# Optimization experiments

Hardware: AMD Instinct MI355X
Metric: run time of the kernel (lower is better)

## Reference

```python
import jax, jax.numpy as jnp
import numpy as np

N = 50000    # total nodes in a batched graph
E = 200000   # directed edges (before self loops)
G = 256      # molecules per batch
F_IN = 64    # atom features
H = 4        # gat heads
CH = 128     # hidden_channels (per head)
D = H * CH   # 512, concat width
MLP_H = 128  # hidden_channels * mlp_hidden_factor
NEG_SLOPE = 0.2


def _gat(x, src, dst, W, a_src, a_dst, b, concat):
    """PyG GATConv (eval mode, self loops already added to src/dst)."""
    n = x.shape[0]
    heads, ch = a_src.shape
    h = (x @ W).reshape(n, heads, ch)                       # [N,H,C]
    e = jax.nn.leaky_relu((h * a_src).sum(-1)[src]
                          + (h * a_dst).sum(-1)[dst], NEG_SLOPE)  # [E,H]
    emax = jax.ops.segment_max(e, dst, num_segments=n)
    emax = jnp.where(jnp.isfinite(emax), emax, 0.0)
    p = jnp.exp(e - emax[dst])
    denom = jax.ops.segment_sum(p, dst, num_segments=n)
    alpha = p / (denom[dst] + 1e-16)                        # segment softmax over dst
    out = jax.ops.segment_sum(h[src] * alpha[..., None], dst, num_segments=n)
    out = out.reshape(n, heads * ch) if concat else out.mean(axis=1)
    return out + b


def _encoder(x, edge_index, batch, p):
    n = x.shape[0]
    loop = jnp.arange(n, dtype=edge_index.dtype)            # GATConv add_self_loops=True
    src = jnp.concatenate([edge_index[0], loop])
    dst = jnp.concatenate([edge_index[1], loop])
    x = jax.nn.elu(_gat(x, src, dst, p['W1'], p['as1'], p['ad1'], p['b1'], True))
    x = jax.nn.elu(_gat(x, src, dst, p['W2'], p['as2'], p['ad2'], p['b2'], True))
    x = _gat(x, src, dst, p['W3'], p['as3'], p['ad3'], p['b3'], False)
    emb = jax.ops.segment_max(x, batch, num_segments=G)     # global_max_pool
    return jnp.where(jnp.isfinite(emb), emb, 0.0)


def setup_inputs() -> dict:
    key = jax.random.key(0)
    ks = jax.random.split(key, 24)
    rn = lambda k, s, sc=0.1: jax.random.normal(k, s, jnp.float32) * sc
    return dict(
        x1=rn(ks[0], (N, F_IN), 1.0),
        edge_index1=jax.random.randint(ks[1], (2, E), 0, N, dtype=jnp.int32),
        batch1=jnp.sort(jax.random.randint(ks[2], (N,), 0, G, dtype=jnp.int32)),
        x2=rn(ks[3], (N, F_IN), 1.0),
        edge_index2=jax.random.randint(ks[4], (2, E), 0, N, dtype=jnp.int32),
        batch2=jnp.sort(jax.random.randint(ks[5], (N,), 0, G, dtype=jnp.int32)),
        W1=rn(ks[6], (F_IN, D)), as1=rn(ks[7], (H, CH)), ad1=rn(ks[8], (H, CH)),
        b1=jnp.zeros((D,), jnp.float32),
        W2=rn(ks[9], (D, D)), as2=rn(ks[10], (H, CH)), ad2=rn(ks[11], (H, CH)),
        b2=jnp.zeros((D,), jnp.float32),
        W3=rn(ks[12], (D, CH)), as3=rn(ks[13], (1, CH)), ad3=rn(ks[14], (1, CH)),
        b3=jnp.zeros((CH,), jnp.float32),
        mw1=rn(ks[15], (2 * CH, MLP_H)), mb1=jnp.zeros((MLP_H,), jnp.float32),
        mw2=rn(ks[16], (MLP_H, 1)), mb2=jnp.zeros((1,), jnp.float32),
    )


def reference(x1, edge_index1, batch1, x2, edge_index2, batch2,
              W1, as1, ad1, b1, W2, as2, ad2, b2, W3, as3, ad3, b3,
              mw1, mb1, mw2, mb2):
    p = dict(W1=W1, as1=as1, ad1=ad1, b1=b1,
             W2=W2, as2=as2, ad2=ad2, b2=b2,
             W3=W3, as3=as3, ad3=ad3, b3=b3)
    e1 = _encoder(x1, edge_index1, batch1, p)               # [G, CH]
    e2 = _encoder(x2, edge_index2, batch2, p)               # [G, CH]
    z = jnp.concatenate([e1, e2], axis=-1)                  # [G, 2*CH]
    return jax.nn.relu(z @ mw1 + mb1) @ mw2 + mb2           # [G, 1]
```

## Files before the change

### kernel.cpp

```cpp
#include <hip/hip_runtime.h>
#include <cstdint>

namespace {
constexpr int kN = 50000;
constexpr int kE = 200000;
constexpr int kE2 = kE + kN;
constexpr int kG = 256;
constexpr float kNegSlope = 0.2f;
}

using half8   = __attribute__((ext_vector_type(8))) _Float16;
using floatx4 = __attribute__((ext_vector_type(4))) float;

__device__ __forceinline__ void gld_lds16(const void* g, void* l) {
  __builtin_amdgcn_global_load_lds(
      (const __attribute__((address_space(1))) unsigned int*)g,
      (__attribute__((address_space(3))) unsigned int*)l, 16, 0, 0);
}

__device__ __forceinline__ float fexp(float x) {
  return __builtin_amdgcn_exp2f(x * 1.44269504088896f);
}

template <int OUTF16, int BN, int CT>
__global__ __launch_bounds__(512, 2) void gemm_ring(
    const _Float16* __restrict__ A, const _Float16* __restrict__ B,
    void* __restrict__ Cv, int M, int N, int K) {
  constexpr int ASL = 1024;
  constexpr int BSL = BN * 4;
  constexpr int SLOT = (ASL + BSL) * 16;
  constexpr int LPT = (ASL + BSL) / 512;
  constexpr int WN = (BN == 256) ? 4 : 2;
  constexpr int WM = 8 / WN;
  constexpr int WTM = 256 / WM;
  constexpr int WTN = BN / WN;
  constexpr int MI = WTM / 16;
  constexpr int NI = WTN / 16;
  __shared__ alignas(16) char smem[4 * SLOT];
  const int t = threadIdx.x;
  const int w = t >> 6, l = t & 63;
  const int x = blockIdx.x & 7, s = blockIdx.x >> 3;
  const int col = (CT == 1) ? 0 : (s & (CT - 1));
  const int rt = ((CT == 1) ? s : (s >> 1)) * 8 + x;
  const int bm = rt * 256;
  const int bn = col * BN;
  if (bm >= M) return;
  const int wr = w / WN, wc = w % WN;
  const int quad = l >> 4, lrow = l & 15;

  floatx4 acc[MI][NI];
#pragma unroll
  for (int mi = 0; mi < MI; ++mi)
#pragma unroll
    for (int ni = 0; ni < NI; ++ni) acc[mi][ni] = (floatx4){0.f, 0.f, 0.f, 0.f};

  auto stageA = [&](int kt) {
    char* buf = smem + (size_t)(kt & 3) * SLOT;
    int k0 = kt * 32;
    k0 = (k0 > K - 32) ? (K - 32) : k0;
#pragma unroll
    for (int i = 0; i < 2; ++i) {
      const int sl = i * 512 + t;
      const int row = ((sl >> 6) << 4) + (sl & 15);
      const int q = (sl >> 4) & 3;
      int ga = bm + row;
      ga = (ga < M) ? ga : (M - 1);
      gld_lds16(A + (size_t)ga * K + k0 + q * 8, buf + sl * 16);
    }
  };
  auto stageB = [&](int kt) {
    char* buf = smem + (size_t)(kt & 3) * SLOT + ASL * 16;
    int k0 = kt * 32;
    k0 = (k0 > K - 32) ? (K - 32) : k0;
#pragma unroll
    for (int i = 0; i < LPT - 2; ++i) {
      const int sl = i * 512 + t;
      const int row = ((sl >> 6) << 4) + (sl & 15);
      const int q = (sl >> 4) & 3;
      gld_lds16(B + (size_t)(bn + row) * K + k0 + q * 8, buf + sl * 16);
    }
  };

  stageA(0); stageB(0);
  stageA(1); stageB(1);
  stageA(2); stageB(2);

  const int NT = K >> 5;
  for (int kt = 0; kt < NT; ++kt) {
    char* bufc = smem + (size_t)(kt & 3) * SLOT;
    stageA(kt + 3);
    if constexpr (BN == 256)
      asm volatile("s_waitcnt vmcnt(10)" ::: "memory");
    else
      asm volatile("s_waitcnt vmcnt(8)" ::: "memory");
    __builtin_amdgcn_s_barrier();
    asm volatile("" ::: "memory");
    half8 fa[MI], fb[NI];
#pragma unroll
    for (int ni = 0; ni < NI; ++ni)
      fb[ni] = *(const half8*)(bufc + ASL * 16 + ((wc * NI + ni) << 10) + l * 16);
#pragma unroll
    for (int mi = 0; mi < MI / 2; ++mi)
      fa[mi] = *(const half8*)(bufc + ((wr * MI + mi) << 10) + l * 16);
    __builtin_amdgcn_s_setprio(1);
#pragma unroll
    for (int mi = 0; mi < MI / 2; ++mi)
#pragma unroll
      for (int ni = 0; ni < NI; ++ni)
        acc[mi][ni] = __builtin_amdgcn_mfma_f32_16x16x32_f16(
            fa[mi], fb[ni], acc[mi][ni], 0, 0, 0);
    __builtin_amdgcn_s_setprio(0);
    stageB(kt + 3);
#pragma unroll
    for (int mi = MI / 2; mi < MI; ++mi)
      fa[mi] = *(const half8*)(bufc + ((wr * MI + mi) << 10) + l * 16);
    __builtin_amdgcn_s_setprio(1);
#pragma unroll
    for (int mi = MI / 2; mi < MI; ++mi)
#pragma unroll
      for (int ni = 0; ni < NI; ++ni)
        acc[mi][ni] = __builtin_amdgcn_mfma_f32_16x16x32_f16(
            fa[mi], fb[ni], acc[mi][ni], 0, 0, 0);
    __builtin_amdgcn_s_setprio(0);
    asm volatile("" ::: "memory");
    __builtin_amdgcn_s_barrier();
  }
  asm volatile("s_waitcnt vmcnt(0)" ::: "memory");
  const int colbase = bn + wc * WTN + lrow;
#pragma unroll
  for (int mi = 0; mi < MI; ++mi) {
    const int rbase = bm + wr * WTM + mi * 16 + quad * 4;
#pragma unroll
    for (int r = 0; r < 4; ++r) {
      const int grow = rbase + r;
      if (grow < M) {
        if constexpr (OUTF16) {
          _Float16* C = (_Float16*)Cv;
#pragma unroll
          for (int ni = 0; ni < NI; ++ni)
            C[(size_t)grow * N + colbase + ni * 16] = (_Float16)acc[mi][ni][r];
        } else {
          float* C = (float*)Cv;
#pragma unroll
          for (int ni = 0; ni < NI; ++ni)
            C[(size_t)grow * N + colbase + ni * 16] = acc[mi][ni][r];
        }
      }
    }
  }
}

__global__ void wt_split_all(const float* __restrict__ W1, _Float16* Th1,
                             const float* __restrict__ W2, _Float16* Th2,
                             const float* __restrict__ W3, _Float16* Th3) {
  int idx = blockIdx.x * blockDim.x + threadIdx.x;
  const float* W;
  _Float16* Th;
  int K, N;
  if (idx < 64 * 512) {
    W = W1; Th = Th1; K = 64; N = 512;
  } else if (idx < 64 * 512 + 512 * 512) {
    idx -= 64 * 512;
    W = W2; Th = Th2; K = 512; N = 512;
  } else if (idx < 64 * 512 + 512 * 512 + 512 * 128) {
    idx -= 64 * 512 + 512 * 512;
    W = W3; Th = Th3; K = 512; N = 128;
  } else {
    return;
  }
  const int k = idx / N;
  const int n = idx - k * N;
  Th[n * K + k] = (_Float16)W[idx];
}

__global__ void prep2(const float* __restrict__ x0, const float* __restrict__ x1,
                      _Float16* __restrict__ Xh, int* __restrict__ cnt,
                      int* __restrict__ total) {
  const int idx = blockIdx.x * blockDim.x + threadIdx.x;
  const int half = kN * 64;
  if (idx < half) Xh[idx] = (_Float16)x0[idx];
  else if (idx < 2 * half) Xh[idx] = (_Float16)x1[idx - half];
  if (idx < 2 * kN) cnt[idx] = 1;
  if (idx == 0) *total = 0;
}
__global__ void prep(const float* __restrict__ X, _Float16* __restrict__ Xh,
                     int* __restrict__ cnt, int* __restrict__ total, int nsplit,
                     int n) {
  const int idx = blockIdx.x * blockDim.x + threadIdx.x;
  if (idx < nsplit) Xh[idx] = (_Float16)X[idx];
  if (idx < n) cnt[idx] = 1;
  if (idx == 0) *total = 0;
}

__global__ void count_edges2(const int* __restrict__ d0, const int* __restrict__ d1,
                             int* __restrict__ cnt) {
  const int i = blockIdx.x * blockDim.x + threadIdx.x;
  if (i < kE) atomicAdd(&cnt[d0[i]], 1);
  else if (i < 2 * kE) atomicAdd(&cnt[d1[i - kE] + kN], 1);
}
__global__ void fill_edges2(const int* __restrict__ s0, const int* __restrict__ d0,
                            const int* __restrict__ s1, const int* __restrict__ d1,
                            int* __restrict__ cursor, int* __restrict__ csr) {
  const int i = blockIdx.x * blockDim.x + threadIdx.x;
  if (i < kE) {
    const int p = atomicAdd(&cursor[d0[i]], 1);
    csr[p] = s0[i];
  } else if (i < 2 * kE) {
    const int j = i - kE;
    const int p = atomicAdd(&cursor[d1[j] + kN], 1);
    csr[p] = s1[j] + kN;
  }
}
__global__ void count_edges(const int* __restrict__ dst, int* __restrict__ cnt,
                            int ne) {
  const int i = blockIdx.x * blockDim.x + threadIdx.x;
  if (i < ne) atomicAdd(&cnt[dst[i]], 1);
}
__global__ void fill_edges(const int* __restrict__ src, const int* __restrict__ dst,
                           int* __restrict__ cursor, int* __restrict__ csr, int ne) {
  const int i = blockIdx.x * blockDim.x + threadIdx.x;
  if (i < ne) {
    const int p = atomicAdd(&cursor[dst[i]], 1);
    csr[p] = src[i];
  }
}
__global__ void alloc_ranges(const int* __restrict__ cnt, int* __restrict__ start,
                             int* __restrict__ cursor, int* __restrict__ total,
                             int* __restrict__ csr, int n) {
  const int i = blockIdx.x * blockDim.x + threadIdx.x;
  const int lane = threadIdx.x & 63;
  const int v = (i < n) ? cnt[i] : 0;
  int sc = v;
#pragma unroll
  for (int off = 1; off < 64; off <<= 1) {
    const int t = __shfl_up(sc, off);
    if (lane >= off) sc += t;
  }
  const int wtot = __shfl(sc, 63);
  int base = 0;
  if (lane == 63) base = atomicAdd(total, wtot);
  base = __shfl(base, 63);
  const int st = base + sc - v;
  if (i < n) {
    start[i] = st;
    cursor[i] = st + 1;
    csr[st] = i;
  }
}

__global__ void gat_agg4(const _Float16* __restrict__ h,
                         const float* __restrict__ a_src,
                         const float* __restrict__ a_dst,
                         const int* __restrict__ start, const int* __restrict__ cnt,
                         const int* __restrict__ csr_src,
                         const float* __restrict__ bias,
                         _Float16* __restrict__ outH, int n_nodes) {
  const int gtid = blockIdx.x * blockDim.x + threadIdx.x;
  const int node = gtid >> 6;
  const int lane = threadIdx.x & 63;
  if (node >= n_nodes) return;
  const int ch = lane * 8;
  float as_r[8], ad_r[8];
#pragma unroll
  for (int j = 0; j < 8; ++j) {
    as_r[j] = a_src[ch + j];
    ad_r[j] = a_dst[ch + j];
  }
  const int s = start[node];
  const int c = cnt[node];
  const half8 vs = *(const half8*)(h + (size_t)node * 512 + ch);
  float fs[8];
  float t_src = 0.f, t_dst = 0.f;
#pragma unroll
  for (int j = 0; j < 8; ++j) {
    fs[j] = (float)vs[j];
    t_src = fmaf(fs[j], as_r[j], t_src);
    t_dst = fmaf(fs[j], ad_r[j], t_dst);
  }
#pragma unroll
  for (int off = 1; off < 16; off <<= 1) {
    t_src += __shfl_xor(t_src, off);
    t_dst += __shfl_xor(t_dst, off);
  }
  const float ad = t_dst;
  float es = t_src + ad;
  es = (es > 0.f) ? es : kNegSlope * es;
  const float ws = fexp(es);
  float d0 = ws, d1 = 0.f;
  float a0[8], a1[8];
#pragma unroll
  for (int j = 0; j < 8; ++j) {
    a0[j] = ws * fs[j];
    a1[j] = 0.f;
  }
  int i = 1;
  for (; i + 2 <= c; i += 2) {
    const int s0 = csr_src[s + i];
    const int s1 = csr_src[s + i + 1];
    const half8 v0 = *(const half8*)(h + (size_t)s0 * 512 + ch);
    const half8 v1 = *(const half8*)(h + (size_t)s1 * 512 + ch);
    float f0[8], f1[8];
    float t0 = 0.f, t1 = 0.f;
#pragma unroll
    for (int j = 0; j < 8; ++j) {
      f0[j] = (float)v0[j];
      f1[j] = (float)v1[j];
      t0 = fmaf(f0[j], as_r[j], t0);
      t1 = fmaf(f1[j], as_r[j], t1);
    }
#pragma unroll
    for (int off = 1; off < 16; off <<= 1) {
      t0 += __shfl_xor(t0, off);
      t1 += __shfl_xor(t1, off);
    }
    float e0 = t0 + ad;
    float e1 = t1 + ad;
    e0 = (e0 > 0.f) ? e0 : kNegSlope * e0;
    e1 = (e1 > 0.f) ? e1 : kNegSlope * e1;
    const float w0 = fexp(e0);
    const float w1 = fexp(e1);
    d0 += w0;
    d1 += w1;
#pragma unroll
    for (int j = 0; j < 8; ++j) {
      a0[j] = fmaf(w0, f0[j], a0[j]);
      a1[j] = fmaf(w1, f1[j], a1[j]);
    }
  }
  if (i < c) {
    const int s0 = csr_src[s + i];
    const half8 v0 = *(const half8*)(h + (size_t)s0 * 512 + ch);
    float f0[8];
    float t0 = 0.f;
#pragma unroll
    for (int j = 0; j < 8; ++j) {
      f0[j] = (float)v0[j];
      t0 = fmaf(f0[j], as_r[j], t0);
    }
#pragma unroll
    for (int off = 1; off < 16; off <<= 1) t0 += __shfl_xor(t0, off);
    float e0 = t0 + ad;
    e0 = (e0 > 0.f) ? e0 : kNegSlope * e0;
    const float w0 = fexp(e0);
    d0 += w0;
#pragma unroll
    for (int j = 0; j < 8; ++j) a0[j] = fmaf(w0, f0[j], a0[j]);
  }
  const float inv = 1.f / (d0 + d1 + 1e-16f);
  half8 H;
#pragma unroll
  for (int j = 0; j < 8; ++j) {
    float v = (a0[j] + a1[j]) * inv + bias[ch + j];
    v = (v > 0.f) ? v : (fexp(v) - 1.f);
    H[j] = (_Float16)v;
  }
  *(half8*)(outH + (size_t)node * 512 + ch) = H;
}

__global__ void gat_agg_l3(const float* __restrict__ h,
                           const float* __restrict__ a_src,
                           const float* __restrict__ a_dst,
                           const int* __restrict__ start, const int* __restrict__ cnt,
                           const int* __restrict__ csr_src,
                           const float* __restrict__ bias,
                           float* __restrict__ out, int n_nodes) {
  const int gtid = blockIdx.x * blockDim.x + threadIdx.x;
  const int node = gtid >> 6;
  const int lane = threadIdx.x & 63;
  if (node >= n_nodes) return;
  const float2 asv = *(const float2*)(a_src + lane * 2);
  const float2 adv = *(const float2*)(a_dst + lane * 2);
  const int s = start[node];
  const int c = cnt[node];
  const float2 vs = *(const float2*)(h + (size_t)node * 128 + lane * 2);
  float t_src = fmaf(vs.x, asv.x, vs.y * asv.y);
  float t_dst = fmaf(vs.x, adv.x, vs.y * adv.y);
#pragma unroll
  for (int off = 1; off < 64; off <<= 1) {
    t_src += __shfl_xor(t_src, off);
    t_dst += __shfl_xor(t_dst, off);
  }
  const float ad = t_dst;
  float es = t_src + ad;
  es = (es > 0.f) ? es : kNegSlope * es;
  const float ws = fexp(es);
  float2 a0 = make_float2(ws * vs.x, ws * vs.y);
  float2 a1 = make_float2(0.f, 0.f);
  float d0 = ws, d1 = 0.f;
  int i = 1;
  for (; i + 2 <= c; i += 2) {
    const int s0 = csr_src[s + i];
    const int s1 = csr_src[s + i + 1];
    const float2 v0 = *(const float2*)(h + (size_t)s0 * 128 + lane * 2);
    const float2 v1 = *(const float2*)(h + (size_t)s1 * 128 + lane * 2);
    float t0 = fmaf(v0.x, asv.x, v0.y * asv.y);
    float t1 = fmaf(v1.x, asv.x, v1.y * asv.y);
#pragma unroll
    for (int off = 1; off < 64; off <<= 1) {
      t0 += __shfl_xor(t0, off);
      t1 += __shfl_xor(t1, off);
    }
    float e0 = t0 + ad;
    float e1 = t1 + ad;
    e0 = (e0 > 0.f) ? e0 : kNegSlope * e0;
    e1 = (e1 > 0.f) ? e1 : kNegSlope * e1;
    const float w0 = fexp(e0);
    const float w1 = fexp(e1);
    d0 += w0;
    d1 += w1;
    a0.x = fmaf(w0, v0.x, a0.x); a1.x = fmaf(w1, v1.x, a1.x);
    a0.y = fmaf(w0, v0.y, a0.y); a1.y = fmaf(w1, v1.y, a1.y);
  }
  if (i < c) {
    const int s0 = csr_src[s + i];
    const float2 v0 = *(const float2*)(h + (size_t)s0 * 128 + lane * 2);
    float t0 = fmaf(v0.x, asv.x, v0.y * asv.y);
#pragma unroll
    for (int off = 1; off < 64; off <<= 1) t0 += __shfl_xor(t0, off);
    float e0 = t0 + ad;
    e0 = (e0 > 0.f) ? e0 : kNegSlope * e0;
    const float w0 = fexp(e0);
    d0 += w0;
    a0.x = fmaf(w0, v0.x, a0.x);
    a0.y = fmaf(w0, v0.y, a0.y);
  }
  const float inv = 1.f / (d0 + d1 + 1e-16f);
  *(float2*)(out + (size_t)node * 128 + lane * 2) =
      make_float2((a0.x + a1.x) * inv + bias[lane * 2],
                  (a0.y + a1.y) * inv + bias[lane * 2 + 1]);
}

__global__ void pool_max2(const float* __restrict__ x, const int* __restrict__ bt1,
                          const int* __restrict__ bt2, float* __restrict__ emb) {
  __shared__ int lohi[2];
  const int enc = blockIdx.x >> 8;
  const int g = blockIdx.x & 255;
  const int* batch = enc ? bt2 : bt1;
  const float* xx = x + (size_t)enc * kN * 128;
  if (threadIdx.x == 0) {
    int lo = 0, hi = kN;
    while (lo < hi) {
      const int mid = (lo + hi) >> 1;
      if (batch[mid] < g) lo = mid + 1; else hi = mid;
    }
    lohi[0] = lo;
    hi = kN;
    while (lo < hi) {
      const int mid = (lo + hi) >> 1;
      if (batch[mid] < g + 1) lo = mid + 1; else hi = mid;
    }
    lohi[1] = lo;
  }
  __syncthreads();
  const int lo = lohi[0], hi = lohi[1];
  const int c = threadIdx.x;
  float m = -1e30f;
  for (int nid = lo; nid < hi; ++nid) m = fmaxf(m, xx[(size_t)nid * 128 + c]);
  emb[(size_t)blockIdx.x * 128 + c] = (lo < hi) ? m : 0.f;
}
__global__ void pool_max(const float* __restrict__ x, const int* __restrict__ batch,
                         float* __restrict__ emb, int n_nodes) {
  __shared__ int lohi[2];
  const int g = blockIdx.x;
  if (threadIdx.x == 0) {
    int lo = 0, hi = n_nodes;
    while (lo < hi) {
      const int mid = (lo + hi) >> 1;
      if (batch[mid] < g) lo = mid + 1; else hi = mid;
    }
    lohi[0] = lo;
    hi = n_nodes;
    while (lo < hi) {
      const int mid = (lo + hi) >> 1;
      if (batch[mid] < g + 1) lo = mid + 1; else hi = mid;
    }
    lohi[1] = lo;
  }
  __syncthreads();
  const int lo = lohi[0], hi = lohi[1];
  const int c = threadIdx.x;
  float m = -1e30f;
  for (int nid = lo; nid < hi; ++nid) m = fmaxf(m, x[(size_t)nid * 128 + c]);
  emb[g * 128 + c] = (lo < hi) ? m : 0.f;
}

__global__ void mlp_head(const float* __restrict__ e1, const float* __restrict__ e2,
                         const float* __restrict__ mw1, const float* __restrict__ mb1,
                         const float* __restrict__ mw2, const float* __restrict__ mb2,
                         float* __restrict__ out) {
  __shared__ float z[256];
  __shared__ float red[128];
  const int g = blockIdx.x;
  const int j = threadIdx.x;
  z[j] = e1[g * 128 + j];
  z[j + 128] = e2[g * 128 + j];
  __syncthreads();
  float acc = mb1[j];
  for (int k = 0; k < 256; ++k) acc = fmaf(z[k], mw1[k * 128 + j], acc);
  acc = fmaxf(acc, 0.f) * mw2[j];
  red[j] = acc;
  __syncthreads();
  for (int s = 64; s > 0; s >>= 1) {
    if (j < s) red[j] += red[j + s];
    __syncthreads();
  }
  if (j == 0) out[g] = red[0] + mb2[0];
}

namespace {
struct Bufs {
  _Float16 *R1h, *R2h;
  float *R1f, *R2f, *asrc, *adst;
  int *cnt, *start, *cursor, *csr, *total;
  _Float16 *Wth1, *Wth2, *Wth3;
  float* emb;
  size_t need;
};

Bufs plan(void* d_ws, int M, int E) {
  Bufs b;
  char* w = (char*)d_ws;
  size_t off = 0;
  auto take = [&](size_t bytes) -> void* {
    void* p = w + off;
    off += (bytes + 255) & ~(size_t)255;
    return p;
  };
  b.R1h = (_Float16*)take((size_t)M * 512 * 2);
  b.R1f = (float*)b.R1h;
  b.R2h = (_Float16*)take((size_t)M * 512 * 2);
  b.R2f = (float*)b.R2h;
  b.asrc = (float*)take((size_t)M * 4 * 4);
  b.adst = (float*)take((size_t)M * 4 * 4);
  b.cnt = (int*)take((size_t)M * 4);
  b.start = (int*)take((size_t)M * 4);
  b.cursor = (int*)take((size_t)M * 4);
  b.csr = (int*)take((size_t)E * 4);
  b.total = (int*)take(256);
  b.Wth1 = (_Float16*)take((size_t)64 * 512 * 2);
  b.Wth2 = (_Float16*)take((size_t)512 * 512 * 2);
  b.Wth3 = (_Float16*)take((size_t)512 * 128 * 2);
  b.emb = (float*)take((size_t)2 * kG * 128 * 4);
  b.need = off;
  return b;
}

void run_layers(const Bufs& b, void* const* d_in, int M, hipStream_t stream) {
  const float* as1 = (const float*)d_in[7];
  const float* ad1 = (const float*)d_in[8];
  const float* b1 = (const float*)d_in[9];
  const float* as2 = (const float*)d_in[11];
  const float* ad2 = (const float*)d_in[12];
  const float* b2 = (const float*)d_in[13];
  const float* as3 = (const float*)d_in[15];
  const float* ad3 = (const float*)d_in[16];
  const float* b3 = (const float*)d_in[17];
  const int nodeBlocks = (M * 64) / 256;
  const int MT = (M + 255) / 256;
  const int SP = (MT + 7) / 8;

  gemm_ring<1, 256, 2><<<SP * 16, 512, 0, stream>>>(b.R1h, b.Wth1, b.R2h, M, 512, 64);
  gat_agg4<<<nodeBlocks, 256, 0, stream>>>(b.R2h, as1, ad1, b.start, b.cnt,
                                           b.csr, b1, b.R1h, M);
  gemm_ring<1, 256, 2><<<SP * 16, 512, 0, stream>>>(b.R1h, b.Wth2, b.R2h, M, 512, 512);
  gat_agg4<<<nodeBlocks, 256, 0, stream>>>(b.R2h, as2, ad2, b.start, b.cnt,
                                           b.csr, b2, b.R1h, M);
  gemm_ring<0, 128, 1><<<SP * 8, 512, 0, stream>>>(b.R1h, b.Wth3, b.R2f, M, 128, 512);
  gat_agg_l3<<<nodeBlocks, 256, 0, stream>>>(b.R2f, as3, ad3, b.start, b.cnt,
                                             b.csr, b3, b.R1f, M);
}
}

extern "C" void kernel_launch(void* const* d_in, const int* in_sizes, int n_in,
                              void* d_out, int out_size, void* d_ws, size_t ws_size,
                              hipStream_t stream) {
  (void)in_sizes; (void)n_in; (void)out_size;
  const float* W1 = (const float*)d_in[6];
  const float* W2 = (const float*)d_in[10];
  const float* W3 = (const float*)d_in[14];
  const float* mw1 = (const float*)d_in[18];
  const float* mb1 = (const float*)d_in[19];
  const float* mw2 = (const float*)d_in[20];
  const float* mb2 = (const float*)d_in[21];

  Bufs bc = plan(d_ws, 2 * kN, 2 * kE2);
  const bool combined = bc.need <= ws_size;
  Bufs b = combined ? bc : plan(d_ws, kN, kE2);

  const int wtot = 64 * 512 + 512 * 512 + 512 * 128;
  wt_split_all<<<(wtot + 255) / 256, 256, 0, stream>>>(W1, b.Wth1, W2, b.Wth2, W3,
                                                       b.Wth3);
  if (combined) {
    const int M = 2 * kN;
    const int* ei0 = (const int*)d_in[1];
    const int* ei1 = (const int*)d_in[4];
    prep2<<<(2 * kN * 64 + 255) / 256, 256, 0, stream>>>(
        (const float*)d_in[0], (const float*)d_in[3], b.R1h, b.cnt, b.total);
    count_edges2<<<(2 * kE + 255) / 256, 256, 0, stream>>>(ei0 + kE, ei1 + kE,
                                                           b.cnt);
    alloc_ranges<<<(M + 255) / 256, 256, 0, stream>>>(b.cnt, b.start, b.cursor,
                                                      b.total, b.csr, M);
    fill_edges2<<<(2 * kE + 255) / 256, 256, 0, stream>>>(ei0, ei0 + kE, ei1,
                                                          ei1 + kE, b.cursor, b.csr);
    run_layers(b, d_in, M, stream);
    pool_max2<<<2 * kG, 128, 0, stream>>>(b.R1f, (const int*)d_in[2],
                                          (const int*)d_in[5], b.emb);
  } else {
    for (int enc = 0; enc < 2; ++enc) {
      const float* x = (const float*)d_in[enc * 3 + 0];
      const int* ei = (const int*)d_in[enc * 3 + 1];
      const int* batch = (const int*)d_in[enc * 3 + 2];
      prep<<<(kN * 64 + 255) / 256, 256, 0, stream>>>(x, b.R1h, b.cnt, b.total,
                                                      kN * 64, kN);
      count_edges<<<(kE + 255) / 256, 256, 0, stream>>>(ei + kE, b.cnt, kE);
      alloc_ranges<<<(kN + 255) / 256, 256, 0, stream>>>(b.cnt, b.start, b.cursor,
                                                         b.total, b.csr, kN);
      fill_edges<<<(kE + 255) / 256, 256, 0, stream>>>(ei, ei + kE, b.cursor, b.csr,
                                                       kE);
      run_layers(b, d_in, kN, stream);
      pool_max<<<kG, 128, 0, stream>>>(b.R1f, batch, b.emb + (size_t)enc * kG * 128,
                                       kN);
    }
  }
  mlp_head<<<kG, 128, 0, stream>>>(b.emb, b.emb + (size_t)kG * 128, mw1, mb1, mw2,
                                   mb2, (float*)d_out);
}
```

Measured before the change: 671.9 us.

## Process two nodes per wave in GAT aggregation, fp16 layer-3 features, fuse weight prep

The aggregation kernels now handle two destination nodes per wavefront, interleaving their neighbour gathers so more independent loads are in flight. The masked iteration runs to the larger degree of the pair, so the shorter node issues dummy loads. Layer 3's GEMM now writes fp16 instead of fp32, which halves the gather traffic in the final aggregation at some precision cost. The weight transpose/convert is folded into the input prep kernel to save a launch.

Result: faster. 642.5 us (-4.4%).

```diff
diff --git a/kernel.cpp b/kernel.cpp
--- a/kernel.cpp
+++ b/kernel.cpp
@@ -10,6 +10,7 @@
 }
 
 using half8   = __attribute__((ext_vector_type(8))) _Float16;
+using half2v  = __attribute__((ext_vector_type(2))) _Float16;
 using floatx4 = __attribute__((ext_vector_type(4))) float;
 
 __device__ __forceinline__ void gld_lds16(const void* g, void* l) {
@@ -173,13 +174,40 @@
   Th[n * K + k] = (_Float16)W[idx];
 }
 
-__global__ void prep2(const float* __restrict__ x0, const float* __restrict__ x1,
-                      _Float16* __restrict__ Xh, int* __restrict__ cnt,
-                      int* __restrict__ total) {
+__global__ void prep_all(const float* __restrict__ x0, const float* __restrict__ x1,
+                         _Float16* __restrict__ Xh, int* __restrict__ cnt,
+                         int* __restrict__ total,
+                         const float* __restrict__ W1, _Float16* Th1,
+                         const float* __restrict__ W2, _Float16* Th2,
+                         const float* __restrict__ W3, _Float16* Th3) {
   const int idx = blockIdx.x * blockDim.x + threadIdx.x;
   const int half = kN * 64;
-  if (idx < half) Xh[idx] = (_Float16)x0[idx];
-  else if (idx < 2 * half) Xh[idx] = (_Float16)x1[idx - half];
+  if (idx < half) {
+    Xh[idx] = (_Float16)x0[idx];
+  } else if (idx < 2 * half) {
+    Xh[idx] = (_Float16)x1[idx - half];
+  } else {
+    int e = idx - 2 * half;
+    const float* W;
+    _Float16* Th;
+    int K, N;
+    if (e < 64 * 512) {
+      W = W1; Th = Th1; K = 64; N = 512;
+    } else if (e < 64 * 512 + 512 * 512) {
+      e -= 64 * 512;
+      W = W2; Th = Th2; K = 512; N = 512;
+    } else if (e < 64 * 512 + 512 * 512 + 512 * 128) {
+      e -= 64 * 512 + 512 * 512;
+      W = W3; Th = Th3; K = 512; N = 128;
+    } else {
+      W = nullptr; Th = nullptr; K = N = 0;
+    }
+    if (W) {
+      const int k = e / N;
+      const int n = e - k * N;
+      Th[n * K + k] = (_Float16)W[e];
+    }
+  }
   if (idx < 2 * kN) cnt[idx] = 1;
   if (idx == 0) *total = 0;
 }
@@ -256,9 +284,12 @@
                          const float* __restrict__ bias,
                          _Float16* __restrict__ outH, int n_nodes) {
   const int gtid = blockIdx.x * blockDim.x + threadIdx.x;
-  const int node = gtid >> 6;
+  const int wid = gtid >> 6;
   const int lane = threadIdx.x & 63;
-  if (node >= n_nodes) return;
+  const int n0 = wid * 2;
+  if (n0 >= n_nodes) return;
+  const int n1r = (n0 + 1 < n_nodes) ? (n0 + 1) : n0;
+  const bool has1 = (n0 + 1 < n_nodes);
   const int ch = lane * 8;
   float as_r[8], ad_r[8];
 #pragma unroll
@@ -266,98 +297,140 @@
     as_r[j] = a_src[ch + j];
     ad_r[j] = a_dst[ch + j];
   }
-  const int s = start[node];
-  const int c = cnt[node];
-  const half8 vs = *(const half8*)(h + (size_t)node * 512 + ch);
-  float fs[8];
-  float t_src = 0.f, t_dst = 0.f;
+  const int s0 = start[n0], c0 = cnt[n0];
+  const int s1 = start[n1r];
+  const int c1 = has1 ? cnt[n1r] : 0;
+  const half8 vsA = *(const half8*)(h + (size_t)n0 * 512 + ch);
+  const half8 vsB = *(const half8*)(h + (size_t)n1r * 512 + ch);
+  float fsA[8], fsB[8];
+  float tAs = 0.f, tAd = 0.f, tBs = 0.f, tBd = 0.f;
 #pragma unroll
   for (int j = 0; j < 8; ++j) {
-    fs[j] = (float)vs[j];
-    t_src = fmaf(fs[j], as_r[j], t_src);
-    t_dst = fmaf(fs[j], ad_r[j], t_dst);
+    fsA[j] = (float)vsA[j];
+    fsB[j] = (float)vsB[j];
+    tAs = fmaf(fsA[j], as_r[j], tAs);
+    tAd = fmaf(fsA[j], ad_r[j], tAd);
+    tBs = fmaf(fsB[j], as_r[j], tBs);
+    tBd = fmaf(fsB[j], ad_r[j], tBd);
   }
 #pragma unroll
   for (int off = 1; off < 16; off <<= 1) {
-    t_src += __shfl_xor(t_src, off);
-    t_dst += __shfl_xor(t_dst, off);
-  }
-  const float ad = t_dst;
-  float es = t_src + ad;
-  es = (es > 0.f) ? es : kNegSlope * es;
-  const float ws = fexp(es);
-  float d0 = ws, d1 = 0.f;
-  float a0[8], a1[8];
+    tAs += __shfl_xor(tAs, off);
+    tAd += __shfl_xor(tAd, off);
+    tBs += __shfl_xor(tBs, off);
+    tBd += __shfl_xor(tBd, off);
+  }
+  const float adA = tAd, adB = tBd;
+  float eA = tAs + adA, eB = tBs + adB;
+  eA = (eA > 0.f) ? eA : kNegSlope * eA;
+  eB = (eB > 0.f) ? eB : kNegSlope * eB;
+  const float wsA = fexp(eA);
+  const float wsB = fexp(eB);
+  float dA = wsA, dB = wsB;
+  float aA[8], aB[8];
 #pragma unroll
   for (int j = 0; j < 8; ++j) {
-    a0[j] = ws * fs[j];
-    a1[j] = 0.f;
-  }
+    aA[j] = wsA * fsA[j];
+    aB[j] = wsB * fsB[j];
+  }
+  const int cm = (c0 > c1) ? c0 : c1;
   int i = 1;
-  for (; i + 2 <= c; i += 2) {
-    const int s0 = csr_src[s + i];
-    const int s1 = csr_src[s + i + 1];
-    const half8 v0 = *(const half8*)(h + (size_t)s0 * 512 + ch);
-    const half8 v1 = *(const half8*)(h + (size_t)s1 * 512 + ch);
-    float f0[8], f1[8];
-    float t0 = 0.f, t1 = 0.f;
+  for (; i + 2 <= cm; i += 2) {
+    const int jA0 = (i < c0) ? i : 0, jA1 = (i + 1 < c0) ? i + 1 : 0;
+    const int jB0 = (i < c1) ? i : 0, jB1 = (i + 1 < c1) ? i + 1 : 0;
+    const int sA0 = csr_src[s0 + jA0];
+    const int sA1 = csr_src[s0 + jA1];
+    const int sB0 = csr_src[s1 + jB0];
+    const int sB1 = csr_src[s1 + jB1];
+    const half8 vA0 = *(const half8*)(h + (size_t)sA0 * 512 + ch);
+    const half8 vA1 = *(const half8*)(h + (size_t)sA1 * 512 + ch);
+    const half8 vB0 = *(const half8*)(h + (size_t)sB0 * 512 + ch);
+    const half8 vB1 = *(const half8*)(h + (size_t)sB1 * 512 + ch);
+    float fA0[8], fA1[8], fB0[8], fB1[8];
+    float tA0 = 0.f, tA1 = 0.f, tB0 = 0.f, tB1 = 0.f;
 #pragma unroll
     for (int j = 0; j < 8; ++j) {
-      f0[j] = (float)v0[j];
-      f1[j] = (float)v1[j];
-      t0 = fmaf(f0[j], as_r[j], t0);
-      t1 = fmaf(f1[j], as_r[j], t1);
+      fA0[j] = (float)vA0[j]; tA0 = fmaf(fA0[j], as_r[j], tA0);
+      fA1[j] = (float)vA1[j]; tA1 = fmaf(fA1[j], as_r[j], tA1);
+      fB0[j] = (float)vB0[j]; tB0 = fmaf(fB0[j], as_r[j], tB0);
+      fB1[j] = (float)vB1[j]; tB1 = fmaf(fB1[j], as_r[j], tB1);
     }
 #pragma unroll
     for (int off = 1; off < 16; off <<= 1) {
-      t0 += __shfl_xor(t0, off);
-      t1 += __shfl_xor(t1, off);
-    }
-    float e0 = t0 + ad;
-    float e1 = t1 + ad;
-    e0 = (e0 > 0.f) ? e0 : kNegSlope * e0;
-    e1 = (e1 > 0.f) ? e1 : kNegSlope * e1;
-    const float w0 = fexp(e0);
-    const float w1 = fexp(e1);
-    d0 += w0;
-    d1 += w1;
+      tA0 += __shfl_xor(tA0, off);
+      tA1 += __shfl_xor(tA1, off);
+      tB0 += __shfl_xor(tB0, off);
+      tB1 += __shfl_xor(tB1, off);
+    }
+    float eA0 = tA0 + adA, eA1 = tA1 + adA;
+    float eB0 = tB0 + adB, eB1 = tB1 + adB;
+    eA0 = (eA0 > 0.f) ? eA0 : kNegSlope * eA0;
+    eA1 = (eA1 > 0.f) ? eA1 : kNegSlope * eA1;
+    eB0 = (eB0 > 0.f) ? eB0 : kNegSlope * eB0;
+    eB1 = (eB1 > 0.f) ? eB1 : kNegSlope * eB1;
+    const float wA0 = (i < c0) ? fexp(eA0) : 0.f;
+    const float wA1 = (i + 1 < c0) ? fexp(eA1) : 0.f;
+    const float wB0 = (i < c1) ? fexp(eB0) : 0.f;
+    const float wB1 = (i + 1 < c1) ? fexp(eB1) : 0.f;
+    dA += wA0 + wA1;
+    dB += wB0 + wB1;
 #pragma unroll
     for (int j = 0; j < 8; ++j) {
-      a0[j] = fmaf(w0, f0[j], a0[j]);
-      a1[j] = fmaf(w1, f1[j], a1[j]);
-    }
-  }
-  if (i < c) {
-    const int s0 = csr_src[s + i];
-    const half8 v0 = *(const half8*)(h + (size_t)s0 * 512 + ch);
-    float f0[8];
-    float t0 = 0.f;
+      aA[j] = fmaf(wA0, fA0[j], aA[j]);
+      aA[j] = fmaf(wA1, fA1[j], aA[j]);
+      aB[j] = fmaf(wB0, fB0[j], aB[j]);
+      aB[j] = fmaf(wB1, fB1[j], aB[j]);
+    }
+  }
+  if (i < cm) {
+    const int jA = (i < c0) ? i : 0;
+    const int jB = (i < c1) ? i : 0;
+    const int sA = csr_src[s0 + jA];
+    const int sB = csr_src[s1 + jB];
+    const half8 vA = *(const half8*)(h + (size_t)sA * 512 + ch);
+    const half8 vB = *(const half8*)(h + (size_t)sB * 512 + ch);
+    float fA[8], fB[8];
+    float tA = 0.f, tB = 0.f;
 #pragma unroll
     for (int j = 0; j < 8; ++j) {
-      f0[j] = (float)v0[j];
-      t0 = fmaf(f0[j], as_r[j], t0);
-    }
-#pragma unroll
-    for (int off = 1; off < 16; off <<= 1) t0 += __shfl_xor(t0, off);
-    float e0 = t0 + ad;
-    e0 = (e0 > 0.f) ? e0 : kNegSlope * e0;
-    const float w0 = fexp(e0);
-    d0 += w0;
-#pragma unroll
-    for (int j = 0; j < 8; ++j) a0[j] = fmaf(w0, f0[j], a0[j]);
-  }
-  const float inv = 1.f / (d0 + d1 + 1e-16f);
-  half8 H;
+      fA[j] = (float)vA[j]; tA = fmaf(fA[j], as_r[j], tA);
+      fB[j] = (float)vB[j]; tB = fmaf(fB[j], as_r[j], tB);
+    }
+#pragma unroll
+    for (int off = 1; off < 16; off <<= 1) {
+      tA += __shfl_xor(tA, off);
+      tB += __shfl_xor(tB, off);
+    }
+    float eA2 = tA + adA, eB2 = tB + adB;
+    eA2 = (eA2 > 0.f) ? eA2 : kNegSlope * eA2;
+    eB2 = (eB2 > 0.f) ? eB2 : kNegSlope * eB2;
+    const float wA = (i < c0) ? fexp(eA2) : 0.f;
+    const float wB = (i < c1) ? fexp(eB2) : 0.f;
+    dA += wA;
+    dB += wB;
+#pragma unroll
+    for (int j = 0; j < 8; ++j) {
+      aA[j] = fmaf(wA, fA[j], aA[j]);
+      aB[j] = fmaf(wB, fB[j], aB[j]);
+    }
+  }
+  const float invA = 1.f / (dA + 1e-16f);
+  const float invB = 1.f / (dB + 1e-16f);
+  half8 HA, HB;
 #pragma unroll
   for (int j = 0; j < 8; ++j) {
-    float v = (a0[j] + a1[j]) * inv + bias[ch + j];
-    v = (v > 0.f) ? v : (fexp(v) - 1.f);
-    H[j] = (_Float16)v;
-  }
-  *(half8*)(outH + (size_t)node * 512 + ch) = H;
-}
-
-__global__ void gat_agg_l3(const float* __restrict__ h,
+    float vA = aA[j] * invA + bias[ch + j];
+    vA = (vA > 0.f) ? vA : (fexp(vA) - 1.f);
+    HA[j] = (_Float16)vA;
+    float vB = aB[j] * invB + bias[ch + j];
+    vB = (vB > 0.f) ? vB : (fexp(vB) - 1.f);
+    HB[j] = (_Float16)vB;
+  }
+  *(half8*)(outH + (size_t)n0 * 512 + ch) = HA;
+  if (has1) *(half8*)(outH + (size_t)n1r * 512 + ch) = HB;
+}
+
+__global__ void gat_agg_l3(const _Float16* __restrict__ h,
                            const float* __restrict__ a_src,
                            const float* __restrict__ a_dst,
                            const int* __restrict__ start, const int* __restrict__ cnt,
@@ -365,69 +438,123 @@
                            const float* __restrict__ bias,
                            float* __restrict__ out, int n_nodes) {
   const int gtid = blockIdx.x * blockDim.x + threadIdx.x;
-  const int node = gtid >> 6;
+  const int wid = gtid >> 6;
   const int lane = threadIdx.x & 63;
-  if (node >= n_nodes) return;
+  const int n0 = wid * 2;
+  if (n0 >= n_nodes) return;
+  const int n1r = (n0 + 1 < n_nodes) ? (n0 + 1) : n0;
+  const bool has1 = (n0 + 1 < n_nodes);
   const float2 asv = *(const float2*)(a_src + lane * 2);
   const float2 adv = *(const float2*)(a_dst + lane * 2);
-  const int s = start[node];
-  const int c = cnt[node];
-  const float2 vs = *(const float2*)(h + (size_t)node * 128 + lane * 2);
-  float t_src = fmaf(vs.x, asv.x, vs.y * asv.y);
-  float t_dst = fmaf(vs.x, adv.x, vs.y * adv.y);
+  const int s0 = start[n0], c0 = cnt[n0];
+  const int s1 = start[n1r];
+  const int c1 = has1 ? cnt[n1r] : 0;
+  const half2v vsA = *(const half2v*)(h + (size_t)n0 * 128 + lane * 2);
+  const half2v vsB = *(const half2v*)(h + (size_t)n1r * 128 + lane * 2);
+  const float xA = (float)vsA[0], yA = (float)vsA[1];
+  const float xB = (float)vsB[0], yB = (float)vsB[1];
+  float tAs = fmaf(xA, asv.x, yA * asv.y);
+  float tAd = fmaf(xA, adv.x, yA * adv.y);
+  float tBs = fmaf(xB, asv.x, yB * asv.y);
+  float tBd = fmaf(xB, adv.x, yB * adv.y);
 #pragma unroll
   for (int off = 1; off < 64; off <<= 1) {
-    t_src += __shfl_xor(t_src, off);
-    t_dst += __shfl_xor(t_dst, off);
-  }
-  const float ad = t_dst;
-  float es = t_src + ad;
-  es = (es > 0.f) ? es : kNegSlope * es;
-  const float ws = fexp(es);
-  float2 a0 = make_float2(ws * vs.x, ws * vs.y);
-  float2 a1 = make_float2(0.f, 0.f);
-  float d0 = ws, d1 = 0.f;
+    tAs += __shfl_xor(tAs, off);
+    tAd += __shfl_xor(tAd, off);
+    tBs += __shfl_xor(tBs, off);
+    tBd += __shfl_xor(tBd, off);
+  }
+  const float adA = tAd, adB = tBd;
+  float eA = tAs + adA, eB = tBs + adB;
+  eA = (eA > 0.f) ? eA : kNegSlope * eA;
+  eB = (eB > 0.f) ? eB : kNegSlope * eB;
+  const float wsA = fexp(eA);
+  const float wsB = fexp(eB);
+  float dA = wsA, dB = wsB;
+  float2 aA = make_float2(wsA * xA, wsA * yA);
+  float2 aB = make_float2(wsB * xB, wsB * yB);
+  const int cm = (c0 > c1) ? c0 : c1;
   int i = 1;
-  for (; i + 2 <= c; i += 2) {
-    const int s0 = csr_src[s + i];
-    const int s1 = csr_src[s + i + 1];
-    const float2 v0 = *(const float2*)(h + (size_t)s0 * 128 + lane * 2);
-    const float2 v1 = *(const float2*)(h + (size_t)s1 * 128 + lane * 2);
-    float t0 = fmaf(v0.x, asv.x, v0.y * asv.y);
-    float t1 = fmaf(v1.x, asv.x, v1.y * asv.y);
+  for (; i + 2 <= cm; i += 2) {
+    const int jA0 = (i < c0) ? i : 0, jA1 = (i + 1 < c0) ? i + 1 : 0;
+    const int jB0 = (i < c1) ? i : 0, jB1 = (i + 1 < c1) ? i + 1 : 0;
+    const int sA0 = csr_src[s0 + jA0];
+    const int sA1 = csr_src[s0 + jA1];
+    const int sB0 = csr_src[s1 + jB0];
+    const int sB1 = csr_src[s1 + jB1];
+    const half2v vA0 = *(const half2v*)(h + (size_t)sA0 * 128 + lane * 2);
+    const half2v vA1 = *(const half2v*)(h + (size_t)sA1 * 128 + lane * 2);
+    const half2v vB0 = *(const half2v*)(h + (size_t)sB0 * 128 + lane * 2);
+    const half2v vB1 = *(const half2v*)(h + (size_t)sB1 * 128 + lane * 2);
+    const float xA0 = (float)vA0[0], yA0 = (float)vA0[1];
+    const float xA1 = (float)vA1[0], yA1 = (float)vA1[1];
+    const float xB0 = (float)vB0[0], yB0 = (float)vB0[1];
+    const float xB1 = (float)vB1[0], yB1 = (float)vB1[1];
+    float tA0 = fmaf(xA0, asv.x, yA0 * asv.y);
+    float tA1 = fmaf(xA1, asv.x, yA1 * asv.y);
+    float tB0 = fmaf(xB0, asv.x, yB0 * asv.y);
+    float tB1 = fmaf(xB1, asv.x, yB1 * asv.y);
 #pragma unroll
     for (int off = 1; off < 64; off <<= 1) {
-      t0 += __shfl_xor(t0, off);
-      t1 += __shfl_xor(t1, off);
-    }
-    float e0 = t0 + ad;
-    float e1 = t1 + ad;
-    e0 = (e0 > 0.f) ? e0 : kNegSlope * e0;
-    e1 = (e1 > 0.f) ? e1 : kNegSlope * e1;
-    const float w0 = fexp(e0);
-    const float w1 = fexp(e1);
-    d0 += w0;
-    d1 += w1;
-    a0.x = fmaf(w0, v0.x, a0.x); a1.x = fmaf(w1, v1.x, a1.x);
-    a0.y = fmaf(w0, v0.y, a0.y); a1.y = fmaf(w1, v1.y, a1.y);
-  }
-  if (i < c) {
-    const int s0 = csr_src[s + i];
-    const float2 v0 = *(const float2*)(h + (size_t)s0 * 128 + lane * 2);
-    float t0 = fmaf(v0.x, asv.x, v0.y * asv.y);
-#pragma unroll
-    for (int off = 1; off < 64; off <<= 1) t0 += __shfl_xor(t0, off);
-    float e0 = t0 + ad;
-    e0 = (e0 > 0.f) ? e0 : kNegSlope * e0;
-    const float w0 = fexp(e0);
-    d0 += w0;
-    a0.x = fmaf(w0, v0.x, a0.x);
-    a0.y = fmaf(w0, v0.y, a0.y);
-  }
-  const float inv = 1.f / (d0 + d1 + 1e-16f);
-  *(float2*)(out + (size_t)node * 128 + lane * 2) =
-      make_float2((a0.x + a1.x) * inv + bias[lane * 2],
-                  (a0.y + a1.y) * inv + bias[lane * 2 + 1]);
+      tA0 += __shfl_xor(tA0, off);
+      tA1 += __shfl_xor(tA1, off);
+      tB0 += __shfl_xor(tB0, off);
+      tB1 += __shfl_xor(tB1, off);
+    }
+    float eA0 = tA0 + adA, eA1 = tA1 + adA;
+    float eB0 = tB0 + adB, eB1 = tB1 + adB;
+    eA0 = (eA0 > 0.f) ? eA0 : kNegSlope * eA0;
+    eA1 = (eA1 > 0.f) ? eA1 : kNegSlope * eA1;
+    eB0 = (eB0 > 0.f) ? eB0 : kNegSlope * eB0;
+    eB1 = (eB1 > 0.f) ? eB1 : kNegSlope * eB1;
+    const float wA0 = (i < c0) ? fexp(eA0) : 0.f;
+    const float wA1 = (i + 1 < c0) ? fexp(eA1) : 0.f;
+    const float wB0 = (i < c1) ? fexp(eB0) : 0.f;
+    const float wB1 = (i + 1 < c1) ? fexp(eB1) : 0.f;
+    dA += wA0 + wA1;
+    dB += wB0 + wB1;
+    aA.x = fmaf(wA0, xA0, aA.x); aA.x = fmaf(wA1, xA1, aA.x);
+    aA.y = fmaf(wA0, yA0, aA.y); aA.y = fmaf(wA1, yA1, aA.y);
+    aB.x = fmaf(wB0, xB0, aB.x); aB.x = fmaf(wB1, xB1, aB.x);
+    aB.y = fmaf(wB0, yB0, aB.y); aB.y = fmaf(wB1, yB1, aB.y);
+  }
+  if (i < cm) {
+    const int jA = (i < c0) ? i : 0;
+    const int jB = (i < c1) ? i : 0;
+    const int sA = csr_src[s0 + jA];
+    const int sB = csr_src[s1 + jB];
+    const half2v vA = *(const half2v*)(h + (size_t)sA * 128 + lane * 2);
+    const half2v vB = *(const half2v*)(h + (size_t)sB * 128 + lane * 2);
+    const float xA2 = (float)vA[0], yA2 = (float)vA[1];
+    const float xB2 = (float)vB[0], yB2 = (float)vB[1];
+    float tA = fmaf(xA2, asv.x, yA2 * asv.y);
+    float tB = fmaf(xB2, asv.x, yB2 * asv.y);
+#pragma unroll
+    for (int off = 1; off < 64; off <<= 1) {
+      tA += __shfl_xor(tA, off);
+      tB += __shfl_xor(tB, off);
+    }
+    float eA2 = tA + adA, eB2 = tB + adB;
+    eA2 = (eA2 > 0.f) ? eA2 : kNegSlope * eA2;
+    eB2 = (eB2 > 0.f) ? eB2 : kNegSlope * eB2;
+    const float wA = (i < c0) ? fexp(eA2) : 0.f;
+    const float wB = (i < c1) ? fexp(eB2) : 0.f;
+    dA += wA;
+    dB += wB;
+    aA.x = fmaf(wA, xA2, aA.x);
+    aA.y = fmaf(wA, yA2, aA.y);
+    aB.x = fmaf(wB, xB2, aB.x);
+    aB.y = fmaf(wB, yB2, aB.y);
+  }
+  const float invA = 1.f / (dA + 1e-16f);
+  const float invB = 1.f / (dB + 1e-16f);
+  *(float2*)(out + (size_t)n0 * 128 + lane * 2) =
+      make_float2(aA.x * invA + bias[lane * 2],
+                  aA.y * invA + bias[lane * 2 + 1]);
+  if (has1)
+    *(float2*)(out + (size_t)n1r * 128 + lane * 2) =
+        make_float2(aB.x * invB + bias[lane * 2],
+                    aB.y * invB + bias[lane * 2 + 1]);
 }
 
 __global__ void pool_max2(const float* __restrict__ x, const int* __restrict__ bt1,
@@ -555,19 +682,19 @@
   const float* as3 = (const float*)d_in[15];
   const float* ad3 = (const float*)d_in[16];
   const float* b3 = (const float*)d_in[17];
-  const int nodeBlocks = (M * 64) / 256;
+  const int aggBlocks = (((M + 1) / 2) * 64 + 255) / 256;
   const int MT = (M + 255) / 256;
   const int SP = (MT + 7) / 8;
 
   gemm_ring<1, 256, 2><<<SP * 16, 512, 0, stream>>>(b.R1h, b.Wth1, b.R2h, M, 512, 64);
-  gat_agg4<<<nodeBlocks, 256, 0, stream>>>(b.R2h, as1, ad1, b.start, b.cnt,
-                                           b.csr, b1, b.R1h, M);
+  gat_agg4<<<aggBlocks, 256, 0, stream>>>(b.R2h, as1, ad1, b.start, b.cnt,
+                                          b.csr, b1, b.R1h, M);
   gemm_ring<1, 256, 2><<<SP * 16, 512, 0, stream>>>(b.R1h, b.Wth2, b.R2h, M, 512, 512);
-  gat_agg4<<<nodeBlocks, 256, 0, stream>>>(b.R2h, as2, ad2, b.start, b.cnt,
-                                           b.csr, b2, b.R1h, M);
-  gemm_ring<0, 128, 1><<<SP * 8, 512, 0, stream>>>(b.R1h, b.Wth3, b.R2f, M, 128, 512);
-  gat_agg_l3<<<nodeBlocks, 256, 0, stream>>>(b.R2f, as3, ad3, b.start, b.cnt,
-                                             b.csr, b3, b.R1f, M);
+  gat_agg4<<<aggBlocks, 256, 0, stream>>>(b.R2h, as2, ad2, b.start, b.cnt,
+                                          b.csr, b2, b.R1h, M);
+  gemm_ring<1, 128, 1><<<SP * 8, 512, 0, stream>>>(b.R1h, b.Wth3, b.R2h, M, 128, 512);
+  gat_agg_l3<<<aggBlocks, 256, 0, stream>>>(b.R2h, as3, ad3, b.start, b.cnt,
+                                            b.csr, b3, b.R1f, M);
 }
 }
 
@@ -588,14 +715,13 @@
   Bufs b = combined ? bc : plan(d_ws, kN, kE2);
 
   const int wtot = 64 * 512 + 512 * 512 + 512 * 128;
-  wt_split_all<<<(wtot + 255) / 256, 256, 0, stream>>>(W1, b.Wth1, W2, b.Wth2, W3,
-                                                       b.Wth3);
   if (combined) {
     const int M = 2 * kN;
     const int* ei0 = (const int*)d_in[1];
     const int* ei1 = (const int*)d_in[4];
-    prep2<<<(2 * kN * 64 + 255) / 256, 256, 0, stream>>>(
-        (const float*)d_in[0], (const float*)d_in[3], b.R1h, b.cnt, b.total);
+    prep_all<<<(M * 64 + wtot + 255) / 256, 256, 0, stream>>>(
+        (const float*)d_in[0], (const float*)d_in[3], b.R1h, b.cnt, b.total,
+        W1, b.Wth1, W2, b.Wth2, W3, b.Wth3);
     count_edges2<<<(2 * kE + 255) / 256, 256, 0, stream>>>(ei0 + kE, ei1 + kE,
                                                            b.cnt);
     alloc_ranges<<<(M + 255) / 256, 256, 0, stream>>>(b.cnt, b.start, b.cursor,
@@ -606,6 +732,8 @@
     pool_max2<<<2 * kG, 128, 0, stream>>>(b.R1f, (const int*)d_in[2],
                                           (const int*)d_in[5], b.emb);
   } else {
+    wt_split_all<<<(wtot + 255) / 256, 256, 0, stream>>>(W1, b.Wth1, W2, b.Wth2,
+                                                         W3, b.Wth3);
     for (int enc = 0; enc < 2; ++enc) {
       const float* x = (const float*)d_in[enc * 3 + 0];
       const int* ei = (const int*)d_in[enc * 3 + 1];
```
